# Optimization experiments

Hardware: AMD Instinct MI355X
Metric: run time of the kernel (lower is better)

## Reference

```python
import jax, jax.numpy as jnp
import numpy as np

EMB = 1024
HEADS = 16

def setup_inputs() -> dict:
    key = jax.random.key(0)
    ks = jax.random.split(key, 5)
    s = 1.0 / np.sqrt(EMB)
    x = jax.random.normal(ks[0], (2, 2048, EMB), dtype=jnp.float32)
    W_qkv = jax.random.normal(ks[1], (EMB, 3 * EMB), dtype=jnp.float32) * s
    b_qkv = jnp.zeros((3 * EMB,), dtype=jnp.float32)
    W_out = jax.random.normal(ks[2], (EMB, EMB), dtype=jnp.float32) * s
    b_out = jnp.zeros((EMB,), dtype=jnp.float32)
    return {"x": x, "W_qkv": W_qkv, "b_qkv": b_qkv, "W_out": W_out, "b_out": b_out}

def reference(x, W_qkv, b_qkv, W_out, b_out):
    B, N, C = x.shape
    H = HEADS
    D = C // H
    qkv = x @ W_qkv + b_qkv                      # [B,N,3C]
    qkv = qkv.reshape(B, N, 3, H, D)
    q, k, v = (qkv[:, :, i].transpose(0, 2, 1, 3) for i in range(3))  # [B,H,N,D]
    # NOTE: original scales by C**-0.5 (full embed dim), not head dim
    scale = C ** (-0.5)
    attn = jnp.einsum('bhnd,bhmd->bhnm', q, k) * scale
    attn = jax.nn.softmax(attn, axis=-1)
    out = jnp.einsum('bhnm,bhmd->bhnd', attn, v)  # [B,H,N,D]
    out = out.transpose(0, 2, 1, 3).reshape(B, N, C)
    return out @ W_out + b_out
```

## Files before the change

### kernel.cpp

```cpp
#include <hip/hip_runtime.h>
#include <hip/hip_bf16.h>
#include <cstdint>
#include <cstddef>

typedef __bf16 bf16;
typedef __bf16 bf16x4 __attribute__((ext_vector_type(4)));
typedef __bf16 bf16x8 __attribute__((ext_vector_type(8)));
typedef float f32x4 __attribute__((ext_vector_type(4)));
typedef float f32x16 __attribute__((ext_vector_type(16)));

#define LOG2E 1.4426950408889634f
#define QSCALE (0.03125f * LOG2E)

#define GLD16(gp, lp)                                                              \
  __builtin_amdgcn_global_load_lds((__attribute__((address_space(1))) void*)(gp),  \
                                   (__attribute__((address_space(3))) void*)(lp),  \
                                   16, 0, 0)

__global__ void k_prep(const float* __restrict__ x, const float* __restrict__ Wqkv,
                       const float* __restrict__ Wout, bf16* __restrict__ xb,
                       bf16* __restrict__ wqT, bf16* __restrict__ woT) {
  const int blk = blockIdx.x, tid = threadIdx.x;
  if (blk < 2048) {
    int i = (blk * 256 + tid) * 8;
    const float4* p = (const float4*)(x + i);
    float4 a = p[0], b = p[1];
    bf16x8 o;
    o[0] = (bf16)a.x; o[1] = (bf16)a.y; o[2] = (bf16)a.z; o[3] = (bf16)a.w;
    o[4] = (bf16)b.x; o[5] = (bf16)b.y; o[6] = (bf16)b.z; o[7] = (bf16)b.w;
    *(bf16x8*)(xb + i) = o;
    return;
  }
  const float* in;
  bf16* out;
  int R = 1024, C, bx, by;
  if (blk < 2048 + 3072) {
    in = Wqkv; out = wqT; C = 3072;
    bx = (blk - 2048) % 96; by = (blk - 2048) / 96;
  } else {
    in = Wout; out = woT; C = 1024;
    bx = (blk - 5120) % 32; by = (blk - 5120) / 32;
  }
  __shared__ float t[32][33];
  const int tx = tid & 31, ty = tid >> 5;
  int c0 = bx * 32, r0 = by * 32;
#pragma unroll
  for (int i = 0; i < 4; i++)
    t[ty + i * 8][tx] = in[(size_t)(r0 + ty + i * 8) * C + c0 + tx];
  __syncthreads();
#pragma unroll
  for (int i = 0; i < 4; i++)
    out[(size_t)(c0 + ty + i * 8) * R + r0 + tx] = (bf16)t[tx][ty + i * 8];
}

__global__ __launch_bounds__(256, 3) void k_gemm_qkv(
    const bf16* __restrict__ A, const bf16* __restrict__ Bt,
    const float* __restrict__ bias,
    bf16* __restrict__ qb, bf16* __restrict__ kb, bf16* __restrict__ vb) {
  __shared__ __align__(16) bf16 As[128 * 32];
  __shared__ __align__(16) bf16 Bs[128 * 32];
  const int tid = threadIdx.x;
  const int lane = tid & 63, w = tid >> 6;
  const int quad = lane >> 4, l16 = lane & 15;
  const int wm = (w >> 1) * 64, wn = (w & 1) * 64;
  const int bm = blockIdx.y * 128, bn = blockIdx.x * 128;
  f32x4 acc[4][4] = {};

  for (int kt = 0; kt < 1024; kt += 32) {
    __syncthreads();
#pragma unroll
    for (int p = 0; p < 2; p++) {
      int idx = p * 256 + tid;
      int row = idx >> 2, bq = idx & 3;
      int gb = (bq - ((row >> 1) & 3)) & 3;
      GLD16(A + (size_t)(bm + row) * 1024 + kt + gb * 8, As + idx * 8);
      GLD16(Bt + (size_t)(bn + row) * 1024 + kt + gb * 8, Bs + idx * 8);
    }
    __syncthreads();

    bf16x8 af[4], bfr[4];
#pragma unroll
    for (int mi = 0; mi < 4; mi++) {
      int row = wm + mi * 16 + l16;
      int bq = (quad + ((row >> 1) & 3)) & 3;
      af[mi] = *(const bf16x8*)(As + row * 32 + bq * 8);
    }
#pragma unroll
    for (int ni = 0; ni < 4; ni++) {
      int row = wn + ni * 16 + l16;
      int bq = (quad + ((row >> 1) & 3)) & 3;
      bfr[ni] = *(const bf16x8*)(Bs + row * 32 + bq * 8);
    }
#pragma unroll
    for (int mi = 0; mi < 4; mi++)
#pragma unroll
      for (int ni = 0; ni < 4; ni++)
        acc[mi][ni] =
            __builtin_amdgcn_mfma_f32_16x16x32_bf16(af[mi], bfr[ni], acc[mi][ni], 0, 0, 0);
  }

#pragma unroll
  for (int ni = 0; ni < 4; ni++) {
    int col = bn + wn + ni * 16 + l16;
    float bv = bias[col];
    int which = col >> 10, cc = col & 1023;
    int h = cc >> 6, d = cc & 63;
    if (which == 2) {
#pragma unroll
      for (int mi = 0; mi < 4; mi++) {
        int rowb = bm + wm + mi * 16 + quad * 4;
        int b = rowb >> 11, n0 = rowb & 2047;
        int n0p = (n0 & ~12) | ((n0 & 4) << 1) | ((n0 & 8) >> 1);
        bf16x4 vv;
#pragma unroll
        for (int r = 0; r < 4; r++) vv[r] = (bf16)(acc[mi][ni][r] + bv);
        *(bf16x4*)(vb + ((size_t)(b * 16 + h) * 64 + d) * 2048 + n0p) = vv;
      }
    } else {
#pragma unroll
      for (int mi = 0; mi < 4; mi++)
#pragma unroll
        for (int r = 0; r < 4; r++) {
          int row = bm + wm + mi * 16 + quad * 4 + r;
          int b = row >> 11, n = row & 2047;
          float v = acc[mi][ni][r] + bv;
          if (which == 0)
            qb[((size_t)(b * 16 + h) * 2048 + n) * 64 + d] = (bf16)(v * QSCALE);
          else
            kb[((size_t)(b * 16 + h) * 2048 + n) * 64 + d] = (bf16)v;
        }
    }
  }
}

__global__ __launch_bounds__(256, 2) void k_gemm_out(
    const bf16* __restrict__ A, const bf16* __restrict__ Bt,
    const float* __restrict__ bias, float* __restrict__ outF) {
  __shared__ __align__(16) bf16 As[64 * 32];
  __shared__ __align__(16) bf16 Bs[128 * 32];
  const int tid = threadIdx.x;
  const int lane = tid & 63, w = tid >> 6;
  const int quad = lane >> 4, l16 = lane & 15;
  const int wm = (w >> 1) * 32, wn = (w & 1) * 64;
  const int cid = (blockIdx.x & 7) * 64 + (blockIdx.x >> 3);
  const int bn = (cid & 7) * 128, bm = (cid >> 3) * 64;
  f32x4 acc[2][4] = {};

  for (int kt = 0; kt < 1024; kt += 32) {
    __syncthreads();
    {
      int idx = tid;
      int row = idx >> 2, bq = idx & 3;
      int gb = (bq - ((row >> 1) & 3)) & 3;
      GLD16(A + (size_t)(bm + row) * 1024 + kt + gb * 8, As + idx * 8);
    }
#pragma unroll
    for (int p = 0; p < 2; p++) {
      int idx = p * 256 + tid;
      int row = idx >> 2, bq = idx & 3;
      int gb = (bq - ((row >> 1) & 3)) & 3;
      GLD16(Bt + (size_t)(bn + row) * 1024 + kt + gb * 8, Bs + idx * 8);
    }
    __syncthreads();

    bf16x8 af[2], bfr[4];
#pragma unroll
    for (int mi = 0; mi < 2; mi++) {
      int row = wm + mi * 16 + l16;
      int bq = (quad + ((row >> 1) & 3)) & 3;
      af[mi] = *(const bf16x8*)(As + row * 32 + bq * 8);
    }
#pragma unroll
    for (int ni = 0; ni < 4; ni++) {
      int row = wn + ni * 16 + l16;
      int bq = (quad + ((row >> 1) & 3)) & 3;
      bfr[ni] = *(const bf16x8*)(Bs + row * 32 + bq * 8);
    }
#pragma unroll
    for (int mi = 0; mi < 2; mi++)
#pragma unroll
      for (int ni = 0; ni < 4; ni++)
        acc[mi][ni] =
            __builtin_amdgcn_mfma_f32_16x16x32_bf16(af[mi], bfr[ni], acc[mi][ni], 0, 0, 0);
  }

#pragma unroll
  for (int ni = 0; ni < 4; ni++) {
    int col = bn + wn + ni * 16 + l16;
    float bv = bias[col];
#pragma unroll
    for (int mi = 0; mi < 2; mi++)
#pragma unroll
      for (int r = 0; r < 4; r++) {
        int row = bm + wm + mi * 16 + quad * 4 + r;
        outF[(size_t)row * 1024 + col] = acc[mi][ni][r] + bv;
      }
  }
}

__global__ __launch_bounds__(256, 2) void k_flash(
    const bf16* __restrict__ Q, const bf16* __restrict__ K,
    const bf16* __restrict__ V, bf16* __restrict__ O) {
  __shared__ __align__(16) bf16 Kt[2][64 * 64];
  __shared__ __align__(16) bf16 Vt[2][64 * 64];
  const int tid = threadIdx.x;
  const int lane = tid & 63, w = tid >> 6;
  const int l31 = lane & 31, h = lane >> 5;
  const int x7 = l31 & 7;
  const int cid = ((blockIdx.x & 7) << 6) | (blockIdx.x >> 3);
  const int qt = cid & 15, bh = cid >> 4;
  const bf16* qh = Q + (size_t)bh * 2048 * 64;
  const bf16* kh = K + (size_t)bh * 2048 * 64;
  const bf16* vh = V + (size_t)bh * 64 * 2048;
  const int qrow = qt * 128 + w * 32 + l31;

  bf16x8 qf[4];
#pragma unroll
  for (int c4 = 0; c4 < 4; c4++)
    qf[c4] = *(const bf16x8*)(qh + (size_t)qrow * 64 + c4 * 16 + h * 8);

  bf16x8 ones;
#pragma unroll
  for (int j = 0; j < 8; j++) ones[j] = (bf16)1.0f;
  f32x16 z16 = {};

  f32x16 o0 = {}, o1 = {};
  f32x16 lacc = {};

  auto stage = [&](int kt2, int buf) {
#pragma unroll
    for (int pp = 0; pp < 2; pp++) {
      int idx = pp * 256 + tid;
      int row = idx >> 3, bq = idx & 7, gb = bq ^ (row & 7);
      GLD16(kh + (size_t)(kt2 * 64 + row) * 64 + gb * 8, &Kt[buf][idx * 8]);
      GLD16(vh + (size_t)row * 2048 + kt2 * 64 + gb * 8, &Vt[buf][idx * 8]);
    }
  };

  stage(0, 0);

  for (int kt2 = 0; kt2 < 32; kt2++) {
    const int p = kt2 & 1;
    __syncthreads();
    if (kt2 < 31) stage(kt2 + 1, p ^ 1);
    const bf16* Kb = &Kt[p][0];
    const bf16* Vb = &Vt[p][0];

    f32x16 a0, a1;
    {
      const bf16* k0 = Kb + l31 * 64;
      const bf16* k1 = k0 + 32 * 64;
      __builtin_amdgcn_s_setprio(1);
#pragma unroll
      for (int c4 = 0; c4 < 4; c4++) {
        int off = ((2 * c4 + h) ^ x7) << 3;
        bf16x8 kf0 = *(const bf16x8*)(k0 + off);
        bf16x8 kf1 = *(const bf16x8*)(k1 + off);
        a0 = __builtin_amdgcn_mfma_f32_32x32x16_bf16(kf0, qf[c4], c4 ? a0 : z16, 0, 0, 0);
        a1 = __builtin_amdgcn_mfma_f32_32x32x16_bf16(kf1, qf[c4], c4 ? a1 : z16, 0, 0, 0);
      }
      __builtin_amdgcn_s_setprio(0);
    }

    const bf16* v0 = Vb + l31 * 64;
    const bf16* v1 = v0 + 32 * 64;

    {
      bf16x8 pf0, pf1;
#pragma unroll
      for (int j = 0; j < 8; j++) {
        pf0[j] = (bf16)__builtin_amdgcn_exp2f(a0[j]);
        pf1[j] = (bf16)__builtin_amdgcn_exp2f(a0[8 + j]);
      }
      int e0 = ((0 + h) ^ x7) << 3, e1 = ((2 + h) ^ x7) << 3;
      bf16x8 vf00 = *(const bf16x8*)(v0 + e0);
      bf16x8 vf10 = *(const bf16x8*)(v1 + e0);
      bf16x8 vf01 = *(const bf16x8*)(v0 + e1);
      bf16x8 vf11 = *(const bf16x8*)(v1 + e1);
      __builtin_amdgcn_s_setprio(1);
      lacc = __builtin_amdgcn_mfma_f32_32x32x16_bf16(ones, pf0, lacc, 0, 0, 0);
      o0 = __builtin_amdgcn_mfma_f32_32x32x16_bf16(vf00, pf0, o0, 0, 0, 0);
      o1 = __builtin_amdgcn_mfma_f32_32x32x16_bf16(vf10, pf0, o1, 0, 0, 0);
      lacc = __builtin_amdgcn_mfma_f32_32x32x16_bf16(ones, pf1, lacc, 0, 0, 0);
      o0 = __builtin_amdgcn_mfma_f32_32x32x16_bf16(vf01, pf1, o0, 0, 0, 0);
      o1 = __builtin_amdgcn_mfma_f32_32x32x16_bf16(vf11, pf1, o1, 0, 0, 0);
      __builtin_amdgcn_s_setprio(0);
    }

    {
      bf16x8 pf2, pf3;
#pragma unroll
      for (int j = 0; j < 8; j++) {
        pf2[j] = (bf16)__builtin_amdgcn_exp2f(a1[j]);
        pf3[j] = (bf16)__builtin_amdgcn_exp2f(a1[8 + j]);
      }
      int e2 = ((4 + h) ^ x7) << 3, e3 = ((6 + h) ^ x7) << 3;
      bf16x8 vf02 = *(const bf16x8*)(v0 + e2);
      bf16x8 vf12 = *(const bf16x8*)(v1 + e2);
      bf16x8 vf03 = *(const bf16x8*)(v0 + e3);
      bf16x8 vf13 = *(const bf16x8*)(v1 + e3);
      __builtin_amdgcn_s_setprio(1);
      lacc = __builtin_amdgcn_mfma_f32_32x32x16_bf16(ones, pf2, lacc, 0, 0, 0);
      o0 = __builtin_amdgcn_mfma_f32_32x32x16_bf16(vf02, pf2, o0, 0, 0, 0);
      o1 = __builtin_amdgcn_mfma_f32_32x32x16_bf16(vf12, pf2, o1, 0, 0, 0);
      lacc = __builtin_amdgcn_mfma_f32_32x32x16_bf16(ones, pf3, lacc, 0, 0, 0);
      o0 = __builtin_amdgcn_mfma_f32_32x32x16_bf16(vf03, pf3, o0, 0, 0, 0);
      o1 = __builtin_amdgcn_mfma_f32_32x32x16_bf16(vf13, pf3, o1, 0, 0, 0);
      __builtin_amdgcn_s_setprio(0);
    }
  }

  float inv = 1.0f / lacc[0];
  const int bb = bh >> 4, hh = bh & 15;
  bf16* orow = O + ((size_t)bb * 2048 + qrow) * 1024 + hh * 64;
#pragma unroll
  for (int g = 0; g < 4; g++) {
    bf16x4 ov0, ov1;
#pragma unroll
    for (int r = 0; r < 4; r++) {
      ov0[r] = (bf16)(o0[4 * g + r] * inv);
      ov1[r] = (bf16)(o1[4 * g + r] * inv);
    }
    *(bf16x4*)(orow + 8 * g + 4 * h) = ov0;
    *(bf16x4*)(orow + 32 + 8 * g + 4 * h) = ov1;
  }
}


extern "C" void kernel_launch(void* const* d_in, const int* in_sizes, int n_in,
                              void* d_out, int out_size, void* d_ws, size_t ws_size,
                              hipStream_t stream) {
  (void)in_sizes; (void)n_in; (void)out_size; (void)ws_size;
  const float* x    = (const float*)d_in[0];
  const float* Wqkv = (const float*)d_in[1];
  const float* bqkv = (const float*)d_in[2];
  const float* Wout = (const float*)d_in[3];
  const float* bout = (const float*)d_in[4];
  float* out = (float*)d_out;

  char* ws = (char*)d_ws;
  size_t off = 0;
  auto take = [&](size_t bytes) {
    char* p = ws + off;
    off += (bytes + 255) & ~(size_t)255;
    return p;
  };
  bf16* xb   = (bf16*)take((size_t)4096 * 1024 * 2);
  bf16* wqT  = (bf16*)take((size_t)3072 * 1024 * 2);
  bf16* woT  = (bf16*)take((size_t)1024 * 1024 * 2);
  bf16* qbuf = (bf16*)take((size_t)32 * 2048 * 64 * 2);
  bf16* kbuf = (bf16*)take((size_t)32 * 2048 * 64 * 2);
  bf16* vbuf = (bf16*)take((size_t)32 * 2048 * 64 * 2);
  bf16* aout = (bf16*)take((size_t)4096 * 1024 * 2);

  k_prep<<<6144, 256, 0, stream>>>(x, Wqkv, Wout, xb, wqT, woT);
  k_gemm_qkv<<<dim3(24, 32), 256, 0, stream>>>(xb, wqT, bqkv, qbuf, kbuf, vbuf);
  k_flash<<<dim3(512), 256, 0, stream>>>(qbuf, kbuf, vbuf, aout);
  k_gemm_out<<<dim3(512), 256, 0, stream>>>(aout, woT, bout, out);
}
```

Before: 177.6 us.

## Triple-buffer LDS tiles with vmcnt-gated barriers in GEMMs and flash attention

Converts the two GEMM kernels from single-buffered synchronous loads to a three-stage LDS pipeline, and the flash kernel from double to triple buffering. Each iteration waits only on the older outstanding global-to-LDS loads via explicit s_waitcnt vmcnt before a raw barrier, so loads for tile t+2 overlap compute on tile t. It also raises wave priority around the MFMA blocks in the GEMMs. The cost is more LDS per block, which may reduce occupancy, especially in k_gemm_qkv with its launch bound of 3 blocks. Correctness depends on the vmcnt counts matching the number of loads issued per stage.

After: 182.7 us. +2.8%, slower.

```diff
diff --git a/kernel.cpp b/kernel.cpp
--- a/kernel.cpp
+++ b/kernel.cpp
@@ -16,6 +16,13 @@
   __builtin_amdgcn_global_load_lds((__attribute__((address_space(1))) void*)(gp),  \
                                    (__attribute__((address_space(3))) void*)(lp),  \
                                    16, 0, 0)
+
+#define PIPE_BARRIER(N)                                        \
+  do {                                                         \
+    asm volatile("s_waitcnt vmcnt(" #N ")" ::: "memory");      \
+    __builtin_amdgcn_s_barrier();                              \
+    asm volatile("" ::: "memory");                             \
+  } while (0)
 
 __global__ void k_prep(const float* __restrict__ x, const float* __restrict__ Wqkv,
                        const float* __restrict__ Wout, bf16* __restrict__ xb,
@@ -57,8 +64,8 @@
     const bf16* __restrict__ A, const bf16* __restrict__ Bt,
     const float* __restrict__ bias,
     bf16* __restrict__ qb, bf16* __restrict__ kb, bf16* __restrict__ vb) {
-  __shared__ __align__(16) bf16 As[128 * 32];
-  __shared__ __align__(16) bf16 Bs[128 * 32];
+  __shared__ __align__(16) bf16 As[3][128 * 32];
+  __shared__ __align__(16) bf16 Bs[3][128 * 32];
   const int tid = threadIdx.x;
   const int lane = tid & 63, w = tid >> 6;
   const int quad = lane >> 4, l16 = lane & 15;
@@ -66,37 +73,47 @@
   const int bm = blockIdx.y * 128, bn = blockIdx.x * 128;
   f32x4 acc[4][4] = {};
 
-  for (int kt = 0; kt < 1024; kt += 32) {
-    __syncthreads();
+  auto stage = [&](int kt, int buf) {
 #pragma unroll
     for (int p = 0; p < 2; p++) {
       int idx = p * 256 + tid;
       int row = idx >> 2, bq = idx & 3;
       int gb = (bq - ((row >> 1) & 3)) & 3;
-      GLD16(A + (size_t)(bm + row) * 1024 + kt + gb * 8, As + idx * 8);
-      GLD16(Bt + (size_t)(bn + row) * 1024 + kt + gb * 8, Bs + idx * 8);
-    }
-    __syncthreads();
+      GLD16(A + (size_t)(bm + row) * 1024 + kt + gb * 8, &As[buf][idx * 8]);
+      GLD16(Bt + (size_t)(bn + row) * 1024 + kt + gb * 8, &Bs[buf][idx * 8]);
+    }
+  };
+
+  stage(0, 0);
+  stage(32, 1);
+
+  for (int t = 0; t < 32; t++) {
+    const int p = t % 3;
+    if (t < 31) PIPE_BARRIER(4);
+    else        PIPE_BARRIER(0);
+    if (t < 30) stage((t + 2) * 32, (t + 2) % 3);
 
     bf16x8 af[4], bfr[4];
 #pragma unroll
     for (int mi = 0; mi < 4; mi++) {
       int row = wm + mi * 16 + l16;
       int bq = (quad + ((row >> 1) & 3)) & 3;
-      af[mi] = *(const bf16x8*)(As + row * 32 + bq * 8);
+      af[mi] = *(const bf16x8*)(&As[p][0] + row * 32 + bq * 8);
     }
 #pragma unroll
     for (int ni = 0; ni < 4; ni++) {
       int row = wn + ni * 16 + l16;
       int bq = (quad + ((row >> 1) & 3)) & 3;
-      bfr[ni] = *(const bf16x8*)(Bs + row * 32 + bq * 8);
-    }
+      bfr[ni] = *(const bf16x8*)(&Bs[p][0] + row * 32 + bq * 8);
+    }
+    __builtin_amdgcn_s_setprio(1);
 #pragma unroll
     for (int mi = 0; mi < 4; mi++)
 #pragma unroll
       for (int ni = 0; ni < 4; ni++)
         acc[mi][ni] =
             __builtin_amdgcn_mfma_f32_16x16x32_bf16(af[mi], bfr[ni], acc[mi][ni], 0, 0, 0);
+    __builtin_amdgcn_s_setprio(0);
   }
 
 #pragma unroll
@@ -136,8 +153,8 @@
 __global__ __launch_bounds__(256, 2) void k_gemm_out(
     const bf16* __restrict__ A, const bf16* __restrict__ Bt,
     const float* __restrict__ bias, float* __restrict__ outF) {
-  __shared__ __align__(16) bf16 As[64 * 32];
-  __shared__ __align__(16) bf16 Bs[128 * 32];
+  __shared__ __align__(16) bf16 As[3][64 * 32];
+  __shared__ __align__(16) bf16 Bs[3][128 * 32];
   const int tid = threadIdx.x;
   const int lane = tid & 63, w = tid >> 6;
   const int quad = lane >> 4, l16 = lane & 15;
@@ -146,42 +163,52 @@
   const int bn = (cid & 7) * 128, bm = (cid >> 3) * 64;
   f32x4 acc[2][4] = {};
 
-  for (int kt = 0; kt < 1024; kt += 32) {
-    __syncthreads();
+  auto stage = [&](int kt, int buf) {
     {
       int idx = tid;
       int row = idx >> 2, bq = idx & 3;
       int gb = (bq - ((row >> 1) & 3)) & 3;
-      GLD16(A + (size_t)(bm + row) * 1024 + kt + gb * 8, As + idx * 8);
+      GLD16(A + (size_t)(bm + row) * 1024 + kt + gb * 8, &As[buf][idx * 8]);
     }
 #pragma unroll
     for (int p = 0; p < 2; p++) {
       int idx = p * 256 + tid;
       int row = idx >> 2, bq = idx & 3;
       int gb = (bq - ((row >> 1) & 3)) & 3;
-      GLD16(Bt + (size_t)(bn + row) * 1024 + kt + gb * 8, Bs + idx * 8);
-    }
-    __syncthreads();
+      GLD16(Bt + (size_t)(bn + row) * 1024 + kt + gb * 8, &Bs[buf][idx * 8]);
+    }
+  };
+
+  stage(0, 0);
+  stage(32, 1);
+
+  for (int t = 0; t < 32; t++) {
+    const int p = t % 3;
+    if (t < 31) PIPE_BARRIER(3);
+    else        PIPE_BARRIER(0);
+    if (t < 30) stage((t + 2) * 32, (t + 2) % 3);
 
     bf16x8 af[2], bfr[4];
 #pragma unroll
     for (int mi = 0; mi < 2; mi++) {
       int row = wm + mi * 16 + l16;
       int bq = (quad + ((row >> 1) & 3)) & 3;
-      af[mi] = *(const bf16x8*)(As + row * 32 + bq * 8);
+      af[mi] = *(const bf16x8*)(&As[p][0] + row * 32 + bq * 8);
     }
 #pragma unroll
     for (int ni = 0; ni < 4; ni++) {
       int row = wn + ni * 16 + l16;
       int bq = (quad + ((row >> 1) & 3)) & 3;
-      bfr[ni] = *(const bf16x8*)(Bs + row * 32 + bq * 8);
-    }
+      bfr[ni] = *(const bf16x8*)(&Bs[p][0] + row * 32 + bq * 8);
+    }
+    __builtin_amdgcn_s_setprio(1);
 #pragma unroll
     for (int mi = 0; mi < 2; mi++)
 #pragma unroll
       for (int ni = 0; ni < 4; ni++)
         acc[mi][ni] =
             __builtin_amdgcn_mfma_f32_16x16x32_bf16(af[mi], bfr[ni], acc[mi][ni], 0, 0, 0);
+    __builtin_amdgcn_s_setprio(0);
   }
 
 #pragma unroll
@@ -201,8 +228,8 @@
 __global__ __launch_bounds__(256, 2) void k_flash(
     const bf16* __restrict__ Q, const bf16* __restrict__ K,
     const bf16* __restrict__ V, bf16* __restrict__ O) {
-  __shared__ __align__(16) bf16 Kt[2][64 * 64];
-  __shared__ __align__(16) bf16 Vt[2][64 * 64];
+  __shared__ __align__(16) bf16 Kt[3][64 * 64];
+  __shared__ __align__(16) bf16 Vt[3][64 * 64];
   const int tid = threadIdx.x;
   const int lane = tid & 63, w = tid >> 6;
   const int l31 = lane & 31, h = lane >> 5;
@@ -238,11 +265,13 @@
   };
 
   stage(0, 0);
+  stage(1, 1);
 
   for (int kt2 = 0; kt2 < 32; kt2++) {
-    const int p = kt2 & 1;
-    __syncthreads();
-    if (kt2 < 31) stage(kt2 + 1, p ^ 1);
+    const int p = kt2 % 3;
+    if (kt2 < 31) PIPE_BARRIER(4);
+    else          PIPE_BARRIER(0);
+    if (kt2 < 30) stage(kt2 + 2, (kt2 + 2) % 3);
     const bf16* Kb = &Kt[p][0];
     const bf16* Vb = &Vt[p][0];
 
```

## Triple-buffer K/V tiles and compute QK^T one tile ahead in flash kernel

Applied to the files above, without the earlier changes.

The flash-attention loop moves from double to triple-buffered K/V shared-memory tiles. It now prefetches two tiles ahead and computes the next tile's QK^T scores while the current tile's softmax-exp and PV MFMAs run. The loop is unrolled by two with ping-pong score accumulators. The aim is to hide LDS-load and MFMA latency between the score and value phases. The cost is more LDS per block and extra accumulator registers, which could limit occupancy.

After: 179.8 us. No clear change (+1.2%).

```diff
diff --git a/kernel.cpp b/kernel.cpp
--- a/kernel.cpp
+++ b/kernel.cpp
@@ -201,8 +201,8 @@
 __global__ __launch_bounds__(256, 2) void k_flash(
     const bf16* __restrict__ Q, const bf16* __restrict__ K,
     const bf16* __restrict__ V, bf16* __restrict__ O) {
-  __shared__ __align__(16) bf16 Kt[2][64 * 64];
-  __shared__ __align__(16) bf16 Vt[2][64 * 64];
+  __shared__ __align__(16) bf16 Kt[3][64 * 64];
+  __shared__ __align__(16) bf16 Vt[3][64 * 64];
   const int tid = threadIdx.x;
   const int lane = tid & 63, w = tid >> 6;
   const int l31 = lane & 31, h = lane >> 5;
@@ -237,40 +237,36 @@
     }
   };
 
-  stage(0, 0);
-
-  for (int kt2 = 0; kt2 < 32; kt2++) {
-    const int p = kt2 & 1;
-    __syncthreads();
-    if (kt2 < 31) stage(kt2 + 1, p ^ 1);
-    const bf16* Kb = &Kt[p][0];
-    const bf16* Vb = &Vt[p][0];
-
-    f32x16 a0, a1;
-    {
-      const bf16* k0 = Kb + l31 * 64;
-      const bf16* k1 = k0 + 32 * 64;
-      __builtin_amdgcn_s_setprio(1);
-#pragma unroll
-      for (int c4 = 0; c4 < 4; c4++) {
-        int off = ((2 * c4 + h) ^ x7) << 3;
-        bf16x8 kf0 = *(const bf16x8*)(k0 + off);
-        bf16x8 kf1 = *(const bf16x8*)(k1 + off);
-        a0 = __builtin_amdgcn_mfma_f32_32x32x16_bf16(kf0, qf[c4], c4 ? a0 : z16, 0, 0, 0);
-        a1 = __builtin_amdgcn_mfma_f32_32x32x16_bf16(kf1, qf[c4], c4 ? a1 : z16, 0, 0, 0);
-      }
-      __builtin_amdgcn_s_setprio(0);
-    }
-
-    const bf16* v0 = Vb + l31 * 64;
+  auto computeS = [&](int buf, f32x16& a0, f32x16& a1) {
+    const bf16* k0 = &Kt[buf][0] + l31 * 64;
+    const bf16* k1 = k0 + 32 * 64;
+    __builtin_amdgcn_s_setprio(1);
+#pragma unroll
+    for (int c4 = 0; c4 < 4; c4++) {
+      int off = ((2 * c4 + h) ^ x7) << 3;
+      bf16x8 kf0 = *(const bf16x8*)(k0 + off);
+      bf16x8 kf1 = *(const bf16x8*)(k1 + off);
+      a0 = __builtin_amdgcn_mfma_f32_32x32x16_bf16(kf0, qf[c4], c4 ? a0 : z16, 0, 0, 0);
+      a1 = __builtin_amdgcn_mfma_f32_32x32x16_bf16(kf1, qf[c4], c4 ? a1 : z16, 0, 0, 0);
+    }
+    __builtin_amdgcn_s_setprio(0);
+  };
+
+  auto iter = [&](int t, f32x16& ac0, f32x16& ac1, f32x16& an0, f32x16& an1) {
+    const int p = t % 3;
+    __syncthreads();
+    if (t < 30) stage(t + 2, (t + 2) % 3);
+    if (t < 31) computeS((t + 1) % 3, an0, an1);
+
+    const bf16* v0 = &Vt[p][0] + l31 * 64;
     const bf16* v1 = v0 + 32 * 64;
 
     {
       bf16x8 pf0, pf1;
 #pragma unroll
       for (int j = 0; j < 8; j++) {
-        pf0[j] = (bf16)__builtin_amdgcn_exp2f(a0[j]);
-        pf1[j] = (bf16)__builtin_amdgcn_exp2f(a0[8 + j]);
+        pf0[j] = (bf16)__builtin_amdgcn_exp2f(ac0[j]);
+        pf1[j] = (bf16)__builtin_amdgcn_exp2f(ac0[8 + j]);
       }
       int e0 = ((0 + h) ^ x7) << 3, e1 = ((2 + h) ^ x7) << 3;
       bf16x8 vf00 = *(const bf16x8*)(v0 + e0);
@@ -291,8 +287,8 @@
       bf16x8 pf2, pf3;
 #pragma unroll
       for (int j = 0; j < 8; j++) {
-        pf2[j] = (bf16)__builtin_amdgcn_exp2f(a1[j]);
-        pf3[j] = (bf16)__builtin_amdgcn_exp2f(a1[8 + j]);
+        pf2[j] = (bf16)__builtin_amdgcn_exp2f(ac1[j]);
+        pf3[j] = (bf16)__builtin_amdgcn_exp2f(ac1[8 + j]);
       }
       int e2 = ((4 + h) ^ x7) << 3, e3 = ((6 + h) ^ x7) << 3;
       bf16x8 vf02 = *(const bf16x8*)(v0 + e2);
@@ -308,6 +304,17 @@
       o1 = __builtin_amdgcn_mfma_f32_32x32x16_bf16(vf13, pf3, o1, 0, 0, 0);
       __builtin_amdgcn_s_setprio(0);
     }
+  };
+
+  stage(0, 0);
+  __syncthreads();
+  stage(1, 1);
+  f32x16 aA0, aA1, aB0, aB1;
+  computeS(0, aA0, aA1);
+
+  for (int t = 0; t < 32; t += 2) {
+    iter(t, aA0, aA1, aB0, aB1);
+    iter(t + 1, aB0, aB1, aA0, aA1);
   }
 
   float inv = 1.0f / lacc[0];
```
